# Kernel tuning notes

Measured on AMD Instinct MI355X. Metric: run time of the kernel, lower is better.

## Reference

```python
import jax, jax.numpy as jnp
import numpy as np
from jax import lax

B, T, SLEN = 65536, 512, 12

def setup_inputs() -> dict:
    key = jax.random.key(0)
    k0, k1, k2 = jax.random.split(key, 3)
    series = jax.random.normal(k0, (B, T), dtype=jnp.float32)
    series_shifts = jax.random.randint(k1, (B,), 0, SLEN)
    init_season = jax.random.uniform(k2, (SLEN,), dtype=jnp.float32)
    return {
        'series': series,
        'series_shifts': series_shifts,
        'alpha': jnp.asarray(0.1, jnp.float32),
        'beta': jnp.asarray(0.1, jnp.float32),
        'gamma': jnp.asarray(0.1, jnp.float32),
        'init_season': init_season,
        'init_trend': jnp.asarray(0.1, jnp.float32),
        'n_preds': 0,  # only runnable value (original code indexes series[:, i] for all i)
    }


def reference(series, series_shifts, alpha, beta, gamma, init_season, init_trend, n_preds):
    # series: (B, T) float32; series_shifts: (B,) int roll amounts
    b, t = series.shape
    slen = init_season.shape[0]
    # Per-batch rolled initial seasonals, as in torch.roll(init_season, shift)
    rolled = jax.vmap(lambda r: jnp.roll(init_season, r))(series_shifts)  # (B, slen)
    # In the original code seasonals[i % slen] always reads the INITIAL rolled
    # seasonal (appended gamma-updates live at indices >= slen and are never read),
    # so the seasonal sequence is fully determined up-front.
    seas = rolled[:, jnp.arange(t) % slen]  # (B, T)

    smooth0 = series[:, 0]                              # (B,)
    trend0 = jnp.full((b,), init_trend, series.dtype)   # (B,)
    res0 = smooth0 + trend0                             # i == 0 output (no seasonal)

    def step(carry, x):
        smooth, trend = carry
        y, season_prev = x  # series[:, i], seasonal at i % slen
        smooth_new = alpha * (y - season_prev) + (1.0 - alpha) * (smooth + trend)
        trend_new = beta * (smooth_new - smooth) + (1.0 - beta) * trend
        res = smooth_new + trend_new + season_prev
        return (smooth_new, trend_new), res

    xs = (series[:, 1:].T, seas[:, 1:].T)  # (T-1, B) each
    _, res_rest = lax.scan(step, (smooth0, trend0), xs)  # (T-1, B)
    result = jnp.concatenate([res0[None, :], res_rest], axis=0).T  # (B, T)
    # n_preds == 0: original returns result[:, -0:] == full series
    return result if n_preds == 0 else result[:, -n_preds:]
```

## Files before the change

kernel.cpp:

```cpp
#include <hip/hip_runtime.h>

#define NB    65536
#define NT    512
#define SLEN  12
#define BLOCK 256
#define ROWS  8
#define CHUNKS 32
#define CLEN  16

__global__ __launch_bounds__(BLOCK) void holtwinters_kernel(
    const float* __restrict__ series,
    const int*   __restrict__ shifts,
    const float* __restrict__ alpha_p,
    const float* __restrict__ beta_p,
    const float* __restrict__ init_season,
    const float* __restrict__ trend0_p,
    float*       __restrict__ out)
{
    __shared__ float  ss[SLEN];
    __shared__ float2 u[CLEN + 1];
    __shared__ float4 Mp[5];

    const int t = threadIdx.x;
    const float alpha  = alpha_p[0];
    const float beta   = beta_p[0];
    const float oma    = 1.0f - alpha;
    const float omb    = 1.0f - beta;
    const float trend0 = trend0_p[0];

    if (t < SLEN) ss[t] = init_season[t];
    if (t == 0) {
        const float a00 = oma, a01 = oma;
        const float a10 = -alpha * beta, a11 = beta * oma + omb;
        float p0 = 1.0f, p1 = 1.0f;
        for (int j = 1; j <= CLEN; ++j) {
            const float q0 = p0 * a00 + p1 * a10;
            const float q1 = p0 * a01 + p1 * a11;
            p0 = q0; p1 = q1;
            u[j] = make_float2(p0, p1);
        }
        float m00 = a00, m01 = a01, m10 = a10, m11 = a11;
        for (int sq = 0; sq < 4; ++sq) {
            const float n00 = m00*m00 + m01*m10;
            const float n01 = m00*m01 + m01*m11;
            const float n10 = m10*m00 + m11*m10;
            const float n11 = m10*m01 + m11*m11;
            m00 = n00; m01 = n01; m10 = n10; m11 = n11;
        }
        for (int d = 0; d < 5; ++d) {
            Mp[d] = make_float4(m00, m01, m10, m11);
            const float n00 = m00*m00 + m01*m10;
            const float n01 = m00*m01 + m01*m11;
            const float n10 = m10*m00 + m11*m10;
            const float n11 = m10*m01 + m11*m11;
            m00 = n00; m01 = n01; m10 = n10; m11 = n11;
        }
    }
    __syncthreads();

    const int r     = t >> 5;
    const int c     = t & 31;
    const int row   = blockIdx.x * ROWS + r;
    const int shift = shifts[row];
    int sidx = ((c * CLEN - shift) % SLEN + SLEN) % SLEN;

    const float* __restrict__ yb = series + (size_t)row * NT + c * CLEN;
    float o[CLEN];
    *(float4*)&o[0]  = *(const float4*)(yb + 0);
    *(float4*)&o[4]  = *(const float4*)(yb + 4);
    *(float4*)&o[8]  = *(const float4*)(yb + 8);
    *(float4*)&o[12] = *(const float4*)(yb + 12);

    float smooth = 0.0f, trend = 0.0f;
    #pragma unroll
    for (int k = 0; k < CLEN; ++k) {
        const float s = ss[sidx];
        sidx = (sidx + 1 == SLEN) ? 0 : sidx + 1;
        const float yy = o[k];
        if (c == 0 && k == 0) {
            smooth = yy;
            trend  = trend0;
            o[0]   = smooth + trend;
        } else {
            const float st = smooth + trend;
            const float sm = alpha * (yy - s) + oma * st;
            trend  = beta * (sm - smooth) + omb * trend;
            smooth = sm;
            o[k]   = sm + trend + s;
        }
    }

    float Ex = smooth, Ey = trend;
    #pragma unroll
    for (int d = 0; d < 5; ++d) {
        const float4 m  = Mp[d];
        const int    dd = 1 << d;
        const float gx = __shfl_up(Ex, dd, CHUNKS);
        const float gy = __shfl_up(Ey, dd, CHUNKS);
        if (c >= dd) {
            Ex += m.x * gx + m.y * gy;
            Ey += m.z * gx + m.w * gy;
        }
    }
    const float Sx = __shfl_up(Ex, 1, CHUNKS);
    const float Sy = __shfl_up(Ey, 1, CHUNKS);

    if (c != 0) {
        #pragma unroll
        for (int k = 0; k < CLEN; ++k) {
            const float2 uk = u[k + 1];
            o[k] += uk.x * Sx + uk.y * Sy;
        }
    }

    float* __restrict__ ob = out + (size_t)row * NT + c * CLEN;
    *(float4*)(ob + 0)  = *(float4*)&o[0];
    *(float4*)(ob + 4)  = *(float4*)&o[4];
    *(float4*)(ob + 8)  = *(float4*)&o[8];
    *(float4*)(ob + 12) = *(float4*)&o[12];
}

extern "C" void kernel_launch(void* const* d_in, const int* in_sizes, int n_in,
                              void* d_out, int out_size, void* d_ws, size_t ws_size,
                              hipStream_t stream) {
    const float* series      = (const float*)d_in[0];
    const int*   shifts      = (const int*)  d_in[1];
    const float* alpha       = (const float*)d_in[2];
    const float* beta        = (const float*)d_in[3];
    const float* init_season = (const float*)d_in[5];
    const float* init_trend  = (const float*)d_in[6];
    float*       out         = (float*)d_out;

    dim3 block(BLOCK);
    dim3 grid(NB / ROWS);
    hipLaunchKernelGGL(holtwinters_kernel, grid, block, 0, stream,
                       series, shifts, alpha, beta, init_season, init_trend, out);
}
```

Baseline: 246.0 us.

## Replace serial chunk recurrence with convolution form and loop rows per block

Each chunk's local recurrence is rewritten as a linear combination of the seasonally adjusted inputs, using precomputed matrix-power coefficients (w, cu, P15). The carry scan then combines chunk end states directly, and outputs are formed by a triangular FMA sum rather than a dependent serial chain. Each block now processes four row groups in a loop, so the per-block coefficient setup is amortised over more rows. This exposes more instruction-level parallelism at the cost of O(CLEN^2) FMAs per chunk and more LDS reads, for a kernel that is likely memory-bound.

```diff
diff --git a/kernel.cpp b/kernel.cpp
--- a/kernel.cpp
+++ b/kernel.cpp
@@ -5,6 +5,7 @@
 #define SLEN  12
 #define BLOCK 256
 #define ROWS  8
+#define ITERS 4
 #define CHUNKS 32
 #define CLEN  16
 
@@ -19,7 +20,10 @@
 {
     __shared__ float  ss[SLEN];
     __shared__ float2 u[CLEN + 1];
+    __shared__ float  cu[CLEN];
+    __shared__ float2 w[CLEN];
     __shared__ float4 Mp[5];
+    __shared__ float4 P15;
 
     const int t = threadIdx.x;
     const float alpha  = alpha_p[0];
@@ -32,23 +36,26 @@
     if (t == 0) {
         const float a00 = oma, a01 = oma;
         const float a10 = -alpha * beta, a11 = beta * oma + omb;
-        float p0 = 1.0f, p1 = 1.0f;
+        float p00 = 1.f, p01 = 0.f, p10 = 0.f, p11 = 1.f;
+        u[0]  = make_float2(1.f, 1.f);
+        cu[0] = 1.0f + beta;
+        w[0]  = make_float2(1.0f, beta);
         for (int j = 1; j <= CLEN; ++j) {
-            const float q0 = p0 * a00 + p1 * a10;
-            const float q1 = p0 * a01 + p1 * a11;
-            p0 = q0; p1 = q1;
-            u[j] = make_float2(p0, p1);
+            const float n00 = p00*a00 + p01*a10;
+            const float n01 = p00*a01 + p01*a11;
+            const float n10 = p10*a00 + p11*a10;
+            const float n11 = p10*a01 + p11*a11;
+            p00 = n00; p01 = n01; p10 = n10; p11 = n11;
+            u[j] = make_float2(p00 + p10, p01 + p11);
+            if (j < CLEN) {
+                cu[j] = (p00 + p10) + beta * (p01 + p11);
+                w[j]  = make_float2(p00 + p01*beta, p10 + p11*beta);
+            }
+            if (j == CLEN - 1) P15 = make_float4(p00, p01, p10, p11);
         }
-        float m00 = a00, m01 = a01, m10 = a10, m11 = a11;
-        for (int sq = 0; sq < 4; ++sq) {
-            const float n00 = m00*m00 + m01*m10;
-            const float n01 = m00*m01 + m01*m11;
-            const float n10 = m10*m00 + m11*m10;
-            const float n11 = m10*m01 + m11*m11;
-            m00 = n00; m01 = n01; m10 = n10; m11 = n11;
-        }
-        for (int d = 0; d < 5; ++d) {
-            Mp[d] = make_float4(m00, m01, m10, m11);
+        float m00 = p00, m01 = p01, m10 = p10, m11 = p11;
+        for (int dlev = 0; dlev < 5; ++dlev) {
+            Mp[dlev] = make_float4(m00, m01, m10, m11);
             const float n00 = m00*m00 + m01*m10;
             const float n01 = m00*m01 + m01*m11;
             const float n10 = m10*m00 + m11*m10;
@@ -58,66 +65,83 @@
     }
     __syncthreads();
 
-    const int r     = t >> 5;
-    const int c     = t & 31;
-    const int row   = blockIdx.x * ROWS + r;
-    const int shift = shifts[row];
-    int sidx = ((c * CLEN - shift) % SLEN + SLEN) % SLEN;
+    const int r = t >> 5;
+    const int c = t & 31;
 
-    const float* __restrict__ yb = series + (size_t)row * NT + c * CLEN;
-    float o[CLEN];
-    *(float4*)&o[0]  = *(const float4*)(yb + 0);
-    *(float4*)&o[4]  = *(const float4*)(yb + 4);
-    *(float4*)&o[8]  = *(const float4*)(yb + 8);
-    *(float4*)&o[12] = *(const float4*)(yb + 12);
+    for (int it = 0; it < ITERS; ++it) {
+        const int row   = (blockIdx.x * ITERS + it) * ROWS + r;
+        const int shift = shifts[row];
+        const int sidx0 = ((c * CLEN - shift) % SLEN + SLEN) % SLEN;
 
-    float smooth = 0.0f, trend = 0.0f;
-    #pragma unroll
-    for (int k = 0; k < CLEN; ++k) {
-        const float s = ss[sidx];
-        sidx = (sidx + 1 == SLEN) ? 0 : sidx + 1;
-        const float yy = o[k];
-        if (c == 0 && k == 0) {
-            smooth = yy;
-            trend  = trend0;
-            o[0]   = smooth + trend;
-        } else {
-            const float st = smooth + trend;
-            const float sm = alpha * (yy - s) + oma * st;
-            trend  = beta * (sm - smooth) + omb * trend;
-            smooth = sm;
-            o[k]   = sm + trend + s;
-        }
-    }
+        const float* __restrict__ yb = series + (size_t)row * NT + c * CLEN;
+        float yv[CLEN];
+        *(float4*)&yv[0]  = *(const float4*)(yb + 0);
+        *(float4*)&yv[4]  = *(const float4*)(yb + 4);
+        *(float4*)&yv[8]  = *(const float4*)(yb + 8);
+        *(float4*)&yv[12] = *(const float4*)(yb + 12);
+        const float y0v = yv[0];
 
-    float Ex = smooth, Ey = trend;
-    #pragma unroll
-    for (int d = 0; d < 5; ++d) {
-        const float4 m  = Mp[d];
-        const int    dd = 1 << d;
-        const float gx = __shfl_up(Ex, dd, CHUNKS);
-        const float gy = __shfl_up(Ey, dd, CHUNKS);
-        if (c >= dd) {
-            Ex += m.x * gx + m.y * gy;
-            Ey += m.z * gx + m.w * gy;
-        }
-    }
-    const float Sx = __shfl_up(Ex, 1, CHUNKS);
-    const float Sy = __shfl_up(Ey, 1, CHUNKS);
-
-    if (c != 0) {
+        float d[CLEN];
+        int sidx = sidx0;
         #pragma unroll
         for (int k = 0; k < CLEN; ++k) {
-            const float2 uk = u[k + 1];
-            o[k] += uk.x * Sx + uk.y * Sy;
+            const float s = ss[sidx];
+            sidx = (sidx + 1 == SLEN) ? 0 : sidx + 1;
+            d[k] = alpha * (yv[k] - s);
         }
+        if (c == 0) d[0] = 0.0f;
+
+        float Ex = 0.f, Ey = 0.f;
+        #pragma unroll
+        for (int j = 0; j < CLEN; ++j) {
+            const float2 wj = w[CLEN - 1 - j];
+            Ex = fmaf(d[j], wj.x, Ex);
+            Ey = fmaf(d[j], wj.y, Ey);
+        }
+        {
+            const float4 p = P15;
+            const float ax = fmaf(p.x, y0v, p.y * trend0);
+            const float ay = fmaf(p.z, y0v, p.w * trend0);
+            if (c == 0) { Ex += ax; Ey += ay; }
+        }
+
+        #pragma unroll
+        for (int dlev = 0; dlev < 5; ++dlev) {
+            const float4 m  = Mp[dlev];
+            const int    dd = 1 << dlev;
+            const float gx = __shfl_up(Ex, dd, CHUNKS);
+            const float gy = __shfl_up(Ey, dd, CHUNKS);
+            if (c >= dd) {
+                Ex = fmaf(m.x, gx, fmaf(m.y, gy, Ex));
+                Ey = fmaf(m.z, gx, fmaf(m.w, gy, Ey));
+            }
+        }
+        float Sx = __shfl_up(Ex, 1, CHUNKS);
+        float Sy = __shfl_up(Ey, 1, CHUNKS);
+        if (c == 0) { Sx = y0v; Sy = trend0; }
+        const int off = (c == 0) ? 0 : 1;
+
+        float o[CLEN];
+        sidx = sidx0;
+        #pragma unroll
+        for (int k = 0; k < CLEN; ++k) {
+            const float s = ss[sidx];
+            sidx = (sidx + 1 == SLEN) ? 0 : sidx + 1;
+            const float2 uk = u[k + off];
+            float acc = fmaf(uk.x, Sx, fmaf(uk.y, Sy, s));
+            #pragma unroll
+            for (int j = 0; j <= k; ++j)
+                acc = fmaf(cu[k - j], d[j], acc);
+            o[k] = acc;
+        }
+        if (c == 0) o[0] = y0v + trend0;
+
+        float* __restrict__ ob = out + (size_t)row * NT + c * CLEN;
+        *(float4*)(ob + 0)  = *(float4*)&o[0];
+        *(float4*)(ob + 4)  = *(float4*)&o[4];
+        *(float4*)(ob + 8)  = *(float4*)&o[8];
+        *(float4*)(ob + 12) = *(float4*)&o[12];
     }
-
-    float* __restrict__ ob = out + (size_t)row * NT + c * CLEN;
-    *(float4*)(ob + 0)  = *(float4*)&o[0];
-    *(float4*)(ob + 4)  = *(float4*)&o[4];
-    *(float4*)(ob + 8)  = *(float4*)&o[8];
-    *(float4*)(ob + 12) = *(float4*)&o[12];
 }
 
 extern "C" void kernel_launch(void* const* d_in, const int* in_sizes, int n_in,
@@ -132,7 +156,7 @@
     float*       out         = (float*)d_out;
 
     dim3 block(BLOCK);
-    dim3 grid(NB / ROWS);
+    dim3 grid(NB / (ROWS * ITERS));
     hipLaunchKernelGGL(holtwinters_kernel, grid, block, 0, stream,
                        series, shifts, alpha, beta, init_season, init_trend, out);
 }
```

New measurement: 260.6 us. 5.9% more time.
